# Kernel optimization log

Measured on AMD Instinct MI355X. Metric: run time of the kernel, lower is better.

Reference implementation:

```python
import jax, jax.numpy as jnp
import numpy as np

NUM_HEADS = 16
HEAD_DIM = 64
WINDOW = 512
D_MODEL = NUM_HEADS * HEAD_DIM
BATCH = 2
SEQ = 2048


def setup_inputs() -> dict:
    key = jax.random.key(0)
    k1, k2, k3 = jax.random.split(key, 3)
    x = jax.random.normal(k1, (BATCH, SEQ, D_MODEL), dtype=jnp.float32)
    # Dense layer params (lecun_normal-like scale for stability)
    qkv_kernel = jax.random.normal(k2, (D_MODEL, 3 * NUM_HEADS * HEAD_DIM), dtype=jnp.float32) / np.sqrt(D_MODEL)
    qkv_bias = jnp.zeros((3 * NUM_HEADS * HEAD_DIM,), dtype=jnp.float32)
    out_kernel = jax.random.normal(k3, (NUM_HEADS * HEAD_DIM, D_MODEL), dtype=jnp.float32) / np.sqrt(D_MODEL)
    out_bias = jnp.zeros((D_MODEL,), dtype=jnp.float32)
    return {"x": x, "qkv_kernel": qkv_kernel, "qkv_bias": qkv_bias,
            "out_kernel": out_kernel, "out_bias": out_bias}


def reference(x, qkv_kernel, qkv_bias, out_kernel, out_bias):
    b, s, d = x.shape
    qkv = x @ qkv_kernel + qkv_bias                       # (b, s, 3*H*hd)
    qkv = qkv.reshape(b, s, 3, NUM_HEADS, HEAD_DIM)
    q = qkv[:, :, 0].transpose(0, 2, 1, 3)                # (b, H, s, hd)
    k = qkv[:, :, 1].transpose(0, 2, 1, 3)
    v = qkv[:, :, 2].transpose(0, 2, 1, 3)
    scale = 1.0 / jnp.sqrt(jnp.float32(HEAD_DIM)).astype(x.dtype)
    scores = jnp.einsum('bhqd,bhkd->bhqk', q, k) * scale  # (b, H, s, s)
    rows = jnp.arange(s)[:, None]
    cols = jnp.arange(s)[None, :]
    window_mask = (rows - cols >= 0) & (rows - cols < WINDOW)
    scores = jnp.where(window_mask[None, None], scores, jnp.asarray(-1e9, scores.dtype))
    attn = jax.nn.softmax(scores, axis=-1)
    out = jnp.einsum('bhqk,bhkd->bhqd', attn, v)          # (b, H, s, hd)
    out = out.transpose(0, 2, 1, 3).reshape(b, s, -1)
    return out @ out_kernel + out_bias
```

## Files before the change

kernel.cpp:

```cpp
#include <hip/hip_runtime.h>
#include <cstdint>
#include <cstddef>

#define NUM_HEADS 16
#define HEAD_DIM  64
#define WINDOW    512
#define D_MODEL   1024
#define BATCH     2
#define SEQ       2048
#define MTOT      (BATCH*SEQ)
#define NQKV      (3*D_MODEL)

typedef short bf16x8 __attribute__((ext_vector_type(8)));
typedef float f32x4  __attribute__((ext_vector_type(4)));

__device__ __forceinline__ f32x4 mfma16(bf16x8 a, bf16x8 b, f32x4 c) {
  return __builtin_amdgcn_mfma_f32_16x16x32_bf16(a, b, c, 0, 0, 0);
}

__device__ __forceinline__ unsigned short f2bf(float f) {
  unsigned int u = __float_as_uint(f);
  u += 0x7fffu + ((u >> 16) & 1u);
  return (unsigned short)(u >> 16);
}
__device__ __forceinline__ float bf2f(unsigned short b) {
  return __uint_as_float(((unsigned int)b) << 16);
}

__device__ __forceinline__ void gld16(const unsigned short* g, unsigned short* l) {
  __builtin_amdgcn_global_load_lds(
      (const __attribute__((address_space(1))) unsigned int*)g,
      (__attribute__((address_space(3))) unsigned int*)l, 16, 0, 0);
}

__global__ __launch_bounds__(256) void cvt_bf16_kernel(const float* __restrict__ in,
                                                       unsigned short* __restrict__ out) {
  int i = (blockIdx.x * 256 + threadIdx.x) * 4;
  float4 v = *(const float4*)(in + i);
  ushort4 o;
  o.x = f2bf(v.x); o.y = f2bf(v.y); o.z = f2bf(v.z); o.w = f2bf(v.w);
  *(ushort4*)(out + i) = o;
}

__global__ __launch_bounds__(256) void transpose_cvt_kernel(const float* __restrict__ in,
                                                            unsigned short* __restrict__ out,
                                                            int R, int C) {
  __shared__ float tile[32][33];
  int tx = threadIdx.x, ty = threadIdx.y;
  int c0 = blockIdx.x * 32, r0 = blockIdx.y * 32;
#pragma unroll
  for (int i = 0; i < 32; i += 8)
    tile[ty + i][tx] = in[(size_t)(r0 + ty + i) * C + c0 + tx];
  __syncthreads();
#pragma unroll
  for (int i = 0; i < 32; i += 8)
    out[(size_t)(c0 + ty + i) * R + r0 + tx] = f2bf(tile[tx][ty + i]);
}

__global__ __launch_bounds__(256) void transpose_v_kernel(const unsigned short* __restrict__ in,
                                                          unsigned short* __restrict__ out) {
  __shared__ unsigned short tile[32][34];
  int tx = threadIdx.x, ty = threadIdx.y;
  int s0 = blockIdx.x * 32, d0 = blockIdx.y * 32, bh = blockIdx.z;
  const unsigned short* ib = in + (size_t)bh * 2048 * 64;
  unsigned short* ob = out + (size_t)bh * 64 * 2048;
#pragma unroll
  for (int i = 0; i < 32; i += 8)
    tile[ty + i][tx] = ib[(size_t)(s0 + ty + i) * 64 + d0 + tx];
  __syncthreads();
#pragma unroll
  for (int i = 0; i < 32; i += 8)
    ob[(size_t)(d0 + ty + i) * 2048 + s0 + tx] = tile[tx][ty + i];
}

__device__ __forceinline__ void gemm_mainloop(const unsigned short* __restrict__ A,
                                              const unsigned short* __restrict__ Bt,
                                              int K, int m0, int n0,
                                              unsigned short* sA, unsigned short* sB,
                                              f32x4 (&acc)[4][4]) {
  const int t = threadIdx.x;
  const int lane = t & 63, wave = t >> 6;
  const int wm = wave >> 1, wn = wave & 1;
  const int lhi = lane >> 4, llo = lane & 15;
  f32x4 zero = {0.f, 0.f, 0.f, 0.f};
#pragma unroll
  for (int i = 0; i < 4; ++i)
#pragma unroll
    for (int j = 0; j < 4; ++j) acc[i][j] = zero;

  const int cswz = (((t & 3) ^ ((t >> 3) & 3)) << 3);
  const unsigned short* gA = A  + (size_t)(m0 + (t >> 2)) * K + cswz;
  const unsigned short* gB = Bt + (size_t)(n0 + (t >> 2)) * K + cswz;
  const size_t rowskip = (size_t)64 * K;
  unsigned short* lA = sA + t * 8;
  unsigned short* lB = sB + t * 8;
  const int rsw = (lhi ^ ((llo >> 1) & 3)) * 8;
  const unsigned short* rA = sA + (wm * 64 + llo) * 32 + rsw;
  const unsigned short* rB = sB + (wn * 64 + llo) * 32 + rsw;

  for (int k0 = 0; k0 < K; k0 += 32) {
    gld16(gA, lA); gld16(gA + rowskip, lA + 2048);
    gld16(gB, lB); gld16(gB + rowskip, lB + 2048);
    gA += 32; gB += 32;
    __syncthreads();
    bf16x8 af[4], bfr[4];
#pragma unroll
    for (int i = 0; i < 4; ++i) af[i]  = *(const bf16x8*)(rA + i * 512);
#pragma unroll
    for (int i = 0; i < 4; ++i) bfr[i] = *(const bf16x8*)(rB + i * 512);
#pragma unroll
    for (int i = 0; i < 4; ++i)
#pragma unroll
      for (int j = 0; j < 4; ++j)
        acc[i][j] = mfma16(af[i], bfr[j], acc[i][j]);
    __syncthreads();
  }
}

__global__ __launch_bounds__(256) void qkv_gemm_kernel(const unsigned short* __restrict__ Xb,
                                                       const unsigned short* __restrict__ Wt,
                                                       const float* __restrict__ bias,
                                                       unsigned short* __restrict__ Qw,
                                                       unsigned short* __restrict__ Kw,
                                                       unsigned short* __restrict__ Vtmp) {
  __shared__ __align__(16) unsigned short sA[128 * 32];
  __shared__ __align__(16) unsigned short sB[128 * 32];
  f32x4 acc[4][4];
  const int m0 = blockIdx.y * 128, n0 = blockIdx.x * 128;
  gemm_mainloop(Xb, Wt, D_MODEL, m0, n0, sA, sB, acc);

  const int t = threadIdx.x, lane = t & 63, wave = t >> 6;
  const int wm = wave >> 1, wn = wave & 1, lhi = lane >> 4, llo = lane & 15;
#pragma unroll
  for (int ti = 0; ti < 4; ++ti) {
#pragma unroll
    for (int tj = 0; tj < 4; ++tj) {
      int n = n0 + wn * 64 + tj * 16 + llo;
      float bv = bias[n];
      int c = n >> 10, h = (n >> 6) & 15, d = n & 63;
#pragma unroll
      for (int r = 0; r < 4; ++r) {
        int m = m0 + wm * 64 + ti * 16 + lhi * 4 + r;
        int b = m >> 11, s = m & 2047;
        int bh = b * 16 + h;
        float v = acc[ti][tj][r] + bv;
        size_t idx = ((size_t)(bh * 2048 + s)) * 64 + d;
        if (c == 0)      Qw[idx]   = f2bf(v * 0.125f);
        else if (c == 1) Kw[idx]   = f2bf(v);
        else             Vtmp[idx] = f2bf(v);
      }
    }
  }
}

__global__ __launch_bounds__(256) void attn_kernel(const unsigned short* __restrict__ Qw,
                                                   const unsigned short* __restrict__ Kw,
                                                   const unsigned short* __restrict__ Vtw,
                                                   unsigned short* __restrict__ AO) {
  __shared__ __align__(16) unsigned short sK[64 * 64];
  __shared__ __align__(16) unsigned short sV[64 * 64];
  __shared__ __align__(16) unsigned short sP[4][16 * 72];
  const int t = threadIdx.x, lane = t & 63, wave = t >> 6;
  const int lhi = lane >> 4, llo = lane & 15;
  const int bh = blockIdx.x;
  const int q0 = (31 - blockIdx.y) << 6;
  const unsigned short* Qb = Qw  + (size_t)bh * 2048 * 64;
  const unsigned short* Kb = Kw  + (size_t)bh * 2048 * 64;
  const unsigned short* Vb = Vtw + (size_t)bh * 64 * 2048;

  const int qrow = q0 + wave * 16 + llo;
  bf16x8 qf0 = *(const bf16x8*)(Qb + (size_t)qrow * 64 + lhi * 8);
  bf16x8 qf1 = *(const bf16x8*)(Qb + (size_t)qrow * 64 + 32 + lhi * 8);

  const int srow = t >> 3;
  const int scol = ((t & 7) ^ (srow & 7)) * 8;
  const int cpos  = (lhi ^ (llo & 7)) * 8;
  const int cposx = cpos ^ 32;

  float m_i = -1e30f, l_i = 0.f;
  f32x4 o[4];
  f32x4 zero = {0.f, 0.f, 0.f, 0.f};
#pragma unroll
  for (int td = 0; td < 4; ++td) o[td] = zero;

  const int kt_lo = (q0 > 511) ? ((q0 - 511) >> 6) : 0;
  const int kt_hi = q0 >> 6;
  for (int kt = kt_lo; kt <= kt_hi; ++kt) {
    const int k0 = kt << 6;
    gld16(Kb + (size_t)(k0 + srow) * 64 + scol,      sK + t * 8);
    gld16(Kb + (size_t)(k0 + srow + 32) * 64 + scol, sK + t * 8 + 2048);
    gld16(Vb + (size_t)srow * 2048 + k0 + scol,        sV + t * 8);
    gld16(Vb + (size_t)(srow + 32) * 2048 + k0 + scol, sV + t * 8 + 2048);
    __syncthreads();

    f32x4 st[4];
#pragma unroll
    for (int tk = 0; tk < 4; ++tk) {
      const unsigned short* kr = sK + (tk * 16 + llo) * 64;
      bf16x8 kf0 = *(const bf16x8*)(kr + cpos);
      bf16x8 kf1 = *(const bf16x8*)(kr + cposx);
      f32x4 z = zero;
      z = mfma16(kf0, qf0, z);
      z = mfma16(kf1, qf1, z);
      st[tk] = z;
    }

    const int kb = k0 + lhi * 4;
    float mx = -1e30f;
#pragma unroll
    for (int tk = 0; tk < 4; ++tk)
#pragma unroll
      for (int r = 0; r < 4; ++r) {
        int key = kb + tk * 16 + r;
        bool ok = (key <= qrow) && (qrow - key < WINDOW);
        float s = ok ? st[tk][r] : -1e30f;
        st[tk][r] = s;
        mx = fmaxf(mx, s);
      }
    mx = fmaxf(mx, __shfl_xor(mx, 16));
    mx = fmaxf(mx, __shfl_xor(mx, 32));
    float mn = fmaxf(m_i, mx);
    float a  = __expf(m_i - mn);
    float rs = 0.f;
    unsigned short* pw = &sP[wave][llo * 72];
#pragma unroll
    for (int tk = 0; tk < 4; ++tk) {
      ushort4 pb;
      pb.x = f2bf(__expf(st[tk][0] - mn));
      pb.y = f2bf(__expf(st[tk][1] - mn));
      pb.z = f2bf(__expf(st[tk][2] - mn));
      pb.w = f2bf(__expf(st[tk][3] - mn));
      *(ushort4*)(pw + tk * 16 + lhi * 4) = pb;
      rs += bf2f(pb.x) + bf2f(pb.y) + bf2f(pb.z) + bf2f(pb.w);
    }
    rs += __shfl_xor(rs, 16);
    rs += __shfl_xor(rs, 32);
    l_i = l_i * a + rs;
    m_i = mn;

    float aR[4];
#pragma unroll
    for (int r = 0; r < 4; ++r) aR[r] = __shfl(a, lhi * 4 + r);
#pragma unroll
    for (int td = 0; td < 4; ++td)
#pragma unroll
      for (int r = 0; r < 4; ++r) o[td][r] *= aR[r];

    bf16x8 pf0 = *(const bf16x8*)(pw + lhi * 8);
    bf16x8 pf1 = *(const bf16x8*)(pw + 32 + lhi * 8);
#pragma unroll
    for (int td = 0; td < 4; ++td) {
      const unsigned short* vr = sV + (td * 16 + llo) * 64;
      bf16x8 vf0 = *(const bf16x8*)(vr + cpos);
      bf16x8 vf1 = *(const bf16x8*)(vr + cposx);
      o[td] = mfma16(pf0, vf0, o[td]);
      o[td] = mfma16(pf1, vf1, o[td]);
    }
    __syncthreads();
  }

  float lR[4];
#pragma unroll
  for (int r = 0; r < 4; ++r) lR[r] = __shfl(l_i, lhi * 4 + r);
  const int b = bh >> 4, h = bh & 15;
#pragma unroll
  for (int td = 0; td < 4; ++td)
#pragma unroll
    for (int r = 0; r < 4; ++r) {
      int qr = q0 + wave * 16 + lhi * 4 + r;
      AO[(size_t)(b * 2048 + qr) * 1024 + h * 64 + td * 16 + llo] = f2bf(o[td][r] / lR[r]);
    }
}

__global__ __launch_bounds__(256) void out_gemm_kernel(const unsigned short* __restrict__ AO,
                                                       const unsigned short* __restrict__ Wt,
                                                       const float* __restrict__ bias,
                                                       float* __restrict__ out) {
  __shared__ __align__(16) unsigned short sA[128 * 32];
  __shared__ __align__(16) unsigned short sB[128 * 32];
  f32x4 acc[4][4];
  const int m0 = blockIdx.y * 128, n0 = blockIdx.x * 128;
  gemm_mainloop(AO, Wt, D_MODEL, m0, n0, sA, sB, acc);

  const int t = threadIdx.x, lane = t & 63, wave = t >> 6;
  const int wm = wave >> 1, wn = wave & 1, lhi = lane >> 4, llo = lane & 15;
#pragma unroll
  for (int ti = 0; ti < 4; ++ti)
#pragma unroll
    for (int tj = 0; tj < 4; ++tj) {
      int n = n0 + wn * 64 + tj * 16 + llo;
      float bv = bias[n];
#pragma unroll
      for (int r = 0; r < 4; ++r) {
        int m = m0 + wm * 64 + ti * 16 + lhi * 4 + r;
        out[(size_t)m * D_MODEL + n] = acc[ti][tj][r] + bv;
      }
    }
}

extern "C" void kernel_launch(void* const* d_in, const int* in_sizes, int n_in,
                              void* d_out, int out_size, void* d_ws, size_t ws_size,
                              hipStream_t stream) {
  const float* x      = (const float*)d_in[0];
  const float* qkv_w  = (const float*)d_in[1];
  const float* qkv_b  = (const float*)d_in[2];
  const float* out_w  = (const float*)d_in[3];
  const float* out_b  = (const float*)d_in[4];
  float* out = (float*)d_out;
  char* ws = (char*)d_ws;

  unsigned short* Xb  = (unsigned short*)(ws);
  unsigned short* Wq  = (unsigned short*)(ws + ((size_t)8  << 20));
  unsigned short* Wo  = (unsigned short*)(ws + ((size_t)14 << 20));
  unsigned short* Qw  = (unsigned short*)(ws + ((size_t)16 << 20));
  unsigned short* Kw  = (unsigned short*)(ws + ((size_t)24 << 20));
  unsigned short* Vtw = (unsigned short*)(ws + ((size_t)32 << 20));
  unsigned short* AO  = (unsigned short*)(ws + ((size_t)40 << 20));

  unsigned short* Vtmp = AO;

  cvt_bf16_kernel<<<MTOT * D_MODEL / 1024, 256, 0, stream>>>(x, Xb);
  transpose_cvt_kernel<<<dim3(NQKV / 32, D_MODEL / 32), dim3(32, 8), 0, stream>>>(qkv_w, Wq, D_MODEL, NQKV);
  transpose_cvt_kernel<<<dim3(D_MODEL / 32, D_MODEL / 32), dim3(32, 8), 0, stream>>>(out_w, Wo, D_MODEL, D_MODEL);
  qkv_gemm_kernel<<<dim3(NQKV / 128, MTOT / 128), 256, 0, stream>>>(Xb, Wq, qkv_b, Qw, Kw, Vtmp);
  transpose_v_kernel<<<dim3(SEQ / 32, HEAD_DIM / 32, BATCH * NUM_HEADS), dim3(32, 8), 0, stream>>>(Vtmp, Vtw);
  attn_kernel<<<dim3(BATCH * NUM_HEADS, SEQ / 64), 256, 0, stream>>>(Qw, Kw, Vtw, AO);
  out_gemm_kernel<<<dim3(D_MODEL / 128, MTOT / 128), 256, 0, stream>>>(AO, Wo, out_b, out);
}
```

Measured before the change: 180.9 us.

## Fuse V transpose into QKV GEMM epilogue and double-buffer 128-row attention tiles

The separate V transpose kernel is removed. The QKV GEMM now writes V directly in transposed layout by swapping the MFMA operands for the V column blocks. The attention kernel handles 128 query rows per block as two 64-row sub-tiles, so each K/V tile is reused across more queries. K/V loads are double-buffered in shared memory to overlap them with compute. This saves a launch and a round trip through memory, at the cost of fewer attention blocks, more registers and LDS, and strided 2-byte stores for V.

After: 190.7 us. +5.4%, slower.

```diff
diff --git a/kernel.cpp b/kernel.cpp
--- a/kernel.cpp
+++ b/kernel.cpp
@@ -57,22 +57,7 @@
     out[(size_t)(c0 + ty + i) * R + r0 + tx] = f2bf(tile[tx][ty + i]);
 }
 
-__global__ __launch_bounds__(256) void transpose_v_kernel(const unsigned short* __restrict__ in,
-                                                          unsigned short* __restrict__ out) {
-  __shared__ unsigned short tile[32][34];
-  int tx = threadIdx.x, ty = threadIdx.y;
-  int s0 = blockIdx.x * 32, d0 = blockIdx.y * 32, bh = blockIdx.z;
-  const unsigned short* ib = in + (size_t)bh * 2048 * 64;
-  unsigned short* ob = out + (size_t)bh * 64 * 2048;
-#pragma unroll
-  for (int i = 0; i < 32; i += 8)
-    tile[ty + i][tx] = ib[(size_t)(s0 + ty + i) * 64 + d0 + tx];
-  __syncthreads();
-#pragma unroll
-  for (int i = 0; i < 32; i += 8)
-    ob[(size_t)(d0 + ty + i) * 2048 + s0 + tx] = tile[tx][ty + i];
-}
-
+template<bool SWAP>
 __device__ __forceinline__ void gemm_mainloop(const unsigned short* __restrict__ A,
                                               const unsigned short* __restrict__ Bt,
                                               int K, int m0, int n0,
@@ -112,7 +97,8 @@
     for (int i = 0; i < 4; ++i)
 #pragma unroll
       for (int j = 0; j < 4; ++j)
-        acc[i][j] = mfma16(af[i], bfr[j], acc[i][j]);
+        acc[i][j] = SWAP ? mfma16(bfr[j], af[i], acc[i][j])
+                         : mfma16(af[i], bfr[j], acc[i][j]);
     __syncthreads();
   }
 }
@@ -122,32 +108,51 @@
                                                        const float* __restrict__ bias,
                                                        unsigned short* __restrict__ Qw,
                                                        unsigned short* __restrict__ Kw,
-                                                       unsigned short* __restrict__ Vtmp) {
+                                                       unsigned short* __restrict__ Vtw) {
   __shared__ __align__(16) unsigned short sA[128 * 32];
   __shared__ __align__(16) unsigned short sB[128 * 32];
   f32x4 acc[4][4];
   const int m0 = blockIdx.y * 128, n0 = blockIdx.x * 128;
-  gemm_mainloop(Xb, Wt, D_MODEL, m0, n0, sA, sB, acc);
-
   const int t = threadIdx.x, lane = t & 63, wave = t >> 6;
   const int wm = wave >> 1, wn = wave & 1, lhi = lane >> 4, llo = lane & 15;
-#pragma unroll
-  for (int ti = 0; ti < 4; ++ti) {
-#pragma unroll
-    for (int tj = 0; tj < 4; ++tj) {
-      int n = n0 + wn * 64 + tj * 16 + llo;
-      float bv = bias[n];
-      int c = n >> 10, h = (n >> 6) & 15, d = n & 63;
-#pragma unroll
-      for (int r = 0; r < 4; ++r) {
-        int m = m0 + wm * 64 + ti * 16 + lhi * 4 + r;
-        int b = m >> 11, s = m & 2047;
+
+  if (n0 < 2048) {
+    gemm_mainloop<false>(Xb, Wt, D_MODEL, m0, n0, sA, sB, acc);
+#pragma unroll
+    for (int ti = 0; ti < 4; ++ti) {
+#pragma unroll
+      for (int tj = 0; tj < 4; ++tj) {
+        int n = n0 + wn * 64 + tj * 16 + llo;
+        float bv = bias[n];
+        int c = n >> 10, h = (n >> 6) & 15, d = n & 63;
+#pragma unroll
+        for (int r = 0; r < 4; ++r) {
+          int m = m0 + wm * 64 + ti * 16 + lhi * 4 + r;
+          int b = m >> 11, s = m & 2047;
+          int bh = b * 16 + h;
+          float v = acc[ti][tj][r] + bv;
+          size_t idx = ((size_t)(bh * 2048 + s)) * 64 + d;
+          if (c == 0) Qw[idx] = f2bf(v * 0.125f);
+          else        Kw[idx] = f2bf(v);
+        }
+      }
+    }
+  } else {
+    gemm_mainloop<true>(Xb, Wt, D_MODEL, m0, n0, sA, sB, acc);
+#pragma unroll
+    for (int ti = 0; ti < 4; ++ti) {
+      int m = m0 + wm * 64 + ti * 16 + llo;
+      int b = m >> 11, s = m & 2047;
+#pragma unroll
+      for (int tj = 0; tj < 4; ++tj) {
+        int nb = n0 + wn * 64 + tj * 16 + lhi * 4;
+        float4 bv = *(const float4*)(bias + nb);
+        int h = (nb >> 6) & 15, dbase = nb & 63;
         int bh = b * 16 + h;
-        float v = acc[ti][tj][r] + bv;
-        size_t idx = ((size_t)(bh * 2048 + s)) * 64 + d;
-        if (c == 0)      Qw[idx]   = f2bf(v * 0.125f);
-        else if (c == 1) Kw[idx]   = f2bf(v);
-        else             Vtmp[idx] = f2bf(v);
+        float bvr[4] = {bv.x, bv.y, bv.z, bv.w};
+#pragma unroll
+        for (int r = 0; r < 4; ++r)
+          Vtw[(size_t)(bh * 64 + dbase + r) * 2048 + s] = f2bf(acc[ti][tj][r] + bvr[r]);
       }
     }
   }
@@ -157,119 +162,151 @@
                                                    const unsigned short* __restrict__ Kw,
                                                    const unsigned short* __restrict__ Vtw,
                                                    unsigned short* __restrict__ AO) {
-  __shared__ __align__(16) unsigned short sK[64 * 64];
-  __shared__ __align__(16) unsigned short sV[64 * 64];
+  __shared__ __align__(16) unsigned short sK[2][64 * 64];
+  __shared__ __align__(16) unsigned short sV[2][64 * 64];
   __shared__ __align__(16) unsigned short sP[4][16 * 72];
   const int t = threadIdx.x, lane = t & 63, wave = t >> 6;
   const int lhi = lane >> 4, llo = lane & 15;
   const int bh = blockIdx.x;
-  const int q0 = (31 - blockIdx.y) << 6;
+  const int q0 = (15 - blockIdx.y) << 7;
   const unsigned short* Qb = Qw  + (size_t)bh * 2048 * 64;
   const unsigned short* Kb = Kw  + (size_t)bh * 2048 * 64;
   const unsigned short* Vb = Vtw + (size_t)bh * 64 * 2048;
 
-  const int qrow = q0 + wave * 16 + llo;
-  bf16x8 qf0 = *(const bf16x8*)(Qb + (size_t)qrow * 64 + lhi * 8);
-  bf16x8 qf1 = *(const bf16x8*)(Qb + (size_t)qrow * 64 + 32 + lhi * 8);
+  const int qrow0 = q0 + wave * 16 + llo;
+  bf16x8 qf[2][2];
+  qf[0][0] = *(const bf16x8*)(Qb + (size_t)qrow0 * 64 + lhi * 8);
+  qf[0][1] = *(const bf16x8*)(Qb + (size_t)qrow0 * 64 + 32 + lhi * 8);
+  qf[1][0] = *(const bf16x8*)(Qb + (size_t)(qrow0 + 64) * 64 + lhi * 8);
+  qf[1][1] = *(const bf16x8*)(Qb + (size_t)(qrow0 + 64) * 64 + 32 + lhi * 8);
 
   const int srow = t >> 3;
   const int scol = ((t & 7) ^ (srow & 7)) * 8;
   const int cpos  = (lhi ^ (llo & 7)) * 8;
   const int cposx = cpos ^ 32;
 
-  float m_i = -1e30f, l_i = 0.f;
-  f32x4 o[4];
+  float m_i[2] = {-1e30f, -1e30f}, l_i[2] = {0.f, 0.f};
+  f32x4 o[2][4];
   f32x4 zero = {0.f, 0.f, 0.f, 0.f};
 #pragma unroll
-  for (int td = 0; td < 4; ++td) o[td] = zero;
+  for (int qs = 0; qs < 2; ++qs)
+#pragma unroll
+    for (int td = 0; td < 4; ++td) o[qs][td] = zero;
 
   const int kt_lo = (q0 > 511) ? ((q0 - 511) >> 6) : 0;
-  const int kt_hi = q0 >> 6;
+  const int kt_hi = (q0 + 64) >> 6;
+
+  {
+    const int k0 = kt_lo << 6;
+    unsigned short* dK = sK[kt_lo & 1];
+    unsigned short* dV = sV[kt_lo & 1];
+    gld16(Kb + (size_t)(k0 + srow) * 64 + scol,      dK + t * 8);
+    gld16(Kb + (size_t)(k0 + srow + 32) * 64 + scol, dK + t * 8 + 2048);
+    gld16(Vb + (size_t)srow * 2048 + k0 + scol,        dV + t * 8);
+    gld16(Vb + (size_t)(srow + 32) * 2048 + k0 + scol, dV + t * 8 + 2048);
+  }
+
   for (int kt = kt_lo; kt <= kt_hi; ++kt) {
+    __syncthreads();
+    if (kt < kt_hi) {
+      const int k0n = (kt + 1) << 6;
+      unsigned short* dK = sK[(kt + 1) & 1];
+      unsigned short* dV = sV[(kt + 1) & 1];
+      gld16(Kb + (size_t)(k0n + srow) * 64 + scol,      dK + t * 8);
+      gld16(Kb + (size_t)(k0n + srow + 32) * 64 + scol, dK + t * 8 + 2048);
+      gld16(Vb + (size_t)srow * 2048 + k0n + scol,        dV + t * 8);
+      gld16(Vb + (size_t)(srow + 32) * 2048 + k0n + scol, dV + t * 8 + 2048);
+    }
+    const unsigned short* bK = sK[kt & 1];
+    const unsigned short* bV = sV[kt & 1];
     const int k0 = kt << 6;
-    gld16(Kb + (size_t)(k0 + srow) * 64 + scol,      sK + t * 8);
-    gld16(Kb + (size_t)(k0 + srow + 32) * 64 + scol, sK + t * 8 + 2048);
-    gld16(Vb + (size_t)srow * 2048 + k0 + scol,        sV + t * 8);
-    gld16(Vb + (size_t)(srow + 32) * 2048 + k0 + scol, sV + t * 8 + 2048);
-    __syncthreads();
-
-    f32x4 st[4];
-#pragma unroll
-    for (int tk = 0; tk < 4; ++tk) {
-      const unsigned short* kr = sK + (tk * 16 + llo) * 64;
-      bf16x8 kf0 = *(const bf16x8*)(kr + cpos);
-      bf16x8 kf1 = *(const bf16x8*)(kr + cposx);
-      f32x4 z = zero;
-      z = mfma16(kf0, qf0, z);
-      z = mfma16(kf1, qf1, z);
-      st[tk] = z;
-    }
-
-    const int kb = k0 + lhi * 4;
-    float mx = -1e30f;
-#pragma unroll
-    for (int tk = 0; tk < 4; ++tk)
+
+#pragma unroll
+    for (int qs = 0; qs < 2; ++qs) {
+      const int qmin = q0 + qs * 64;
+      if (k0 > qmin + 63 || k0 + 63 < qmin - (WINDOW - 1)) continue;
+      const int qrow = qrow0 + qs * 64;
+
+      f32x4 st[4];
+#pragma unroll
+      for (int tk = 0; tk < 4; ++tk) {
+        const unsigned short* kr = bK + (tk * 16 + llo) * 64;
+        bf16x8 kf0 = *(const bf16x8*)(kr + cpos);
+        bf16x8 kf1 = *(const bf16x8*)(kr + cposx);
+        f32x4 z = zero;
+        z = mfma16(kf0, qf[qs][0], z);
+        z = mfma16(kf1, qf[qs][1], z);
+        st[tk] = z;
+      }
+
+      const int kb = k0 + lhi * 4;
+      float mx = -1e30f;
+#pragma unroll
+      for (int tk = 0; tk < 4; ++tk)
+#pragma unroll
+        for (int r = 0; r < 4; ++r) {
+          int key = kb + tk * 16 + r;
+          bool ok = (key <= qrow) && (qrow - key < WINDOW);
+          float s = ok ? st[tk][r] : -1e30f;
+          st[tk][r] = s;
+          mx = fmaxf(mx, s);
+        }
+      mx = fmaxf(mx, __shfl_xor(mx, 16));
+      mx = fmaxf(mx, __shfl_xor(mx, 32));
+      float mn = fmaxf(m_i[qs], mx);
+      float a  = __expf(m_i[qs] - mn);
+      float rs = 0.f;
+      unsigned short* pw = &sP[wave][llo * 72];
+#pragma unroll
+      for (int tk = 0; tk < 4; ++tk) {
+        ushort4 pb;
+        pb.x = f2bf(__expf(st[tk][0] - mn));
+        pb.y = f2bf(__expf(st[tk][1] - mn));
+        pb.z = f2bf(__expf(st[tk][2] - mn));
+        pb.w = f2bf(__expf(st[tk][3] - mn));
+        *(ushort4*)(pw + tk * 16 + lhi * 4) = pb;
+        rs += bf2f(pb.x) + bf2f(pb.y) + bf2f(pb.z) + bf2f(pb.w);
+      }
+      rs += __shfl_xor(rs, 16);
+      rs += __shfl_xor(rs, 32);
+      l_i[qs] = l_i[qs] * a + rs;
+      m_i[qs] = mn;
+
+      float aR[4];
+#pragma unroll
+      for (int r = 0; r < 4; ++r) aR[r] = __shfl(a, lhi * 4 + r);
+#pragma unroll
+      for (int td = 0; td < 4; ++td)
+#pragma unroll
+        for (int r = 0; r < 4; ++r) o[qs][td][r] *= aR[r];
+
+      bf16x8 pf0 = *(const bf16x8*)(pw + lhi * 8);
+      bf16x8 pf1 = *(const bf16x8*)(pw + 32 + lhi * 8);
+#pragma unroll
+      for (int td = 0; td < 4; ++td) {
+        const unsigned short* vr = bV + (td * 16 + llo) * 64;
+        bf16x8 vf0 = *(const bf16x8*)(vr + cpos);
+        bf16x8 vf1 = *(const bf16x8*)(vr + cposx);
+        o[qs][td] = mfma16(pf0, vf0, o[qs][td]);
+        o[qs][td] = mfma16(pf1, vf1, o[qs][td]);
+      }
+    }
+  }
+
+  const int b = bh >> 4, h = bh & 15;
+#pragma unroll
+  for (int qs = 0; qs < 2; ++qs) {
+    float lR[4];
+#pragma unroll
+    for (int r = 0; r < 4; ++r) lR[r] = 1.f / __shfl(l_i[qs], lhi * 4 + r);
+#pragma unroll
+    for (int td = 0; td < 4; ++td)
 #pragma unroll
       for (int r = 0; r < 4; ++r) {
-        int key = kb + tk * 16 + r;
-        bool ok = (key <= qrow) && (qrow - key < WINDOW);
-        float s = ok ? st[tk][r] : -1e30f;
-        st[tk][r] = s;
-        mx = fmaxf(mx, s);
-      }
-    mx = fmaxf(mx, __shfl_xor(mx, 16));
-    mx = fmaxf(mx, __shfl_xor(mx, 32));
-    float mn = fmaxf(m_i, mx);
-    float a  = __expf(m_i - mn);
-    float rs = 0.f;
-    unsigned short* pw = &sP[wave][llo * 72];
-#pragma unroll
-    for (int tk = 0; tk < 4; ++tk) {
-      ushort4 pb;
-      pb.x = f2bf(__expf(st[tk][0] - mn));
-      pb.y = f2bf(__expf(st[tk][1] - mn));
-      pb.z = f2bf(__expf(st[tk][2] - mn));
-      pb.w = f2bf(__expf(st[tk][3] - mn));
-      *(ushort4*)(pw + tk * 16 + lhi * 4) = pb;
-      rs += bf2f(pb.x) + bf2f(pb.y) + bf2f(pb.z) + bf2f(pb.w);
-    }
-    rs += __shfl_xor(rs, 16);
-    rs += __shfl_xor(rs, 32);
-    l_i = l_i * a + rs;
-    m_i = mn;
-
-    float aR[4];
-#pragma unroll
-    for (int r = 0; r < 4; ++r) aR[r] = __shfl(a, lhi * 4 + r);
-#pragma unroll
-    for (int td = 0; td < 4; ++td)
-#pragma unroll
-      for (int r = 0; r < 4; ++r) o[td][r] *= aR[r];
-
-    bf16x8 pf0 = *(const bf16x8*)(pw + lhi * 8);
-    bf16x8 pf1 = *(const bf16x8*)(pw + 32 + lhi * 8);
-#pragma unroll
-    for (int td = 0; td < 4; ++td) {
-      const unsigned short* vr = sV + (td * 16 + llo) * 64;
-      bf16x8 vf0 = *(const bf16x8*)(vr + cpos);
-      bf16x8 vf1 = *(const bf16x8*)(vr + cposx);
-      o[td] = mfma16(pf0, vf0, o[td]);
-      o[td] = mfma16(pf1, vf1, o[td]);
-    }
-    __syncthreads();
-  }
-
-  float lR[4];
-#pragma unroll
-  for (int r = 0; r < 4; ++r) lR[r] = __shfl(l_i, lhi * 4 + r);
-  const int b = bh >> 4, h = bh & 15;
-#pragma unroll
-  for (int td = 0; td < 4; ++td)
-#pragma unroll
-    for (int r = 0; r < 4; ++r) {
-      int qr = q0 + wave * 16 + lhi * 4 + r;
-      AO[(size_t)(b * 2048 + qr) * 1024 + h * 64 + td * 16 + llo] = f2bf(o[td][r] / lR[r]);
-    }
+        int qr = q0 + qs * 64 + wave * 16 + lhi * 4 + r;
+        AO[(size_t)(b * 2048 + qr) * 1024 + h * 64 + td * 16 + llo] = f2bf(o[qs][td][r] * lR[r]);
+      }
+  }
 }
 
 __global__ __launch_bounds__(256) void out_gemm_kernel(const unsigned short* __restrict__ AO,
@@ -280,7 +317,7 @@
   __shared__ __align__(16) unsigned short sB[128 * 32];
   f32x4 acc[4][4];
   const int m0 = blockIdx.y * 128, n0 = blockIdx.x * 128;
-  gemm_mainloop(AO, Wt, D_MODEL, m0, n0, sA, sB, acc);
+  gemm_mainloop<false>(AO, Wt, D_MODEL, m0, n0, sA, sB, acc);
 
   const int t = threadIdx.x, lane = t & 63, wave = t >> 6;
   const int wm = wave >> 1, wn = wave & 1, lhi = lane >> 4, llo = lane & 15;
@@ -317,13 +354,10 @@
   unsigned short* Vtw = (unsigned short*)(ws + ((size_t)32 << 20));
   unsigned short* AO  = (unsigned short*)(ws + ((size_t)40 << 20));
 
-  unsigned short* Vtmp = AO;
-
   cvt_bf16_kernel<<<MTOT * D_MODEL / 1024, 256, 0, stream>>>(x, Xb);
   transpose_cvt_kernel<<<dim3(NQKV / 32, D_MODEL / 32), dim3(32, 8), 0, stream>>>(qkv_w, Wq, D_MODEL, NQKV);
   transpose_cvt_kernel<<<dim3(D_MODEL / 32, D_MODEL / 32), dim3(32, 8), 0, stream>>>(out_w, Wo, D_MODEL, D_MODEL);
-  qkv_gemm_kernel<<<dim3(NQKV / 128, MTOT / 128), 256, 0, stream>>>(Xb, Wq, qkv_b, Qw, Kw, Vtmp);
-  transpose_v_kernel<<<dim3(SEQ / 32, HEAD_DIM / 32, BATCH * NUM_HEADS), dim3(32, 8), 0, stream>>>(Vtmp, Vtw);
-  attn_kernel<<<dim3(BATCH * NUM_HEADS, SEQ / 64), 256, 0, stream>>>(Qw, Kw, Vtw, AO);
+  qkv_gemm_kernel<<<dim3(NQKV / 128, MTOT / 128), 256, 0, stream>>>(Xb, Wq, qkv_b, Qw, Kw, Vtw);
+  attn_kernel<<<dim3(BATCH * NUM_HEADS, SEQ / 128), 256, 0, stream>>>(Qw, Kw, Vtw, AO);
   out_gemm_kernel<<<dim3(D_MODEL / 128, MTOT / 128), 256, 0, stream>>>(AO, Wo, out_b, out);
 }
```
